# Optimization experiments

Measured on AMD Instinct MI355X. Metric: run time of the kernel, lower is better.

## Reference

```python
import jax, jax.numpy as jnp
import numpy as np

HIDDEN = 128

def setup_inputs() -> dict:
    key = jax.random.key(0)
    ks = jax.random.split(key, 7)
    B, T, I, O = 256, 512, 256, 1000
    s_ih = 1.0 / np.sqrt(HIDDEN)
    x = jax.random.normal(ks[0], (B, T, I), dtype=jnp.float32)
    W_ih = jax.random.uniform(ks[1], (HIDDEN, I), minval=-s_ih, maxval=s_ih, dtype=jnp.float32)
    W_hh = jax.random.uniform(ks[2], (HIDDEN, HIDDEN), minval=-s_ih, maxval=s_ih, dtype=jnp.float32)
    b_ih = jax.random.uniform(ks[3], (HIDDEN,), minval=-s_ih, maxval=s_ih, dtype=jnp.float32)
    b_hh = jax.random.uniform(ks[4], (HIDDEN,), minval=-s_ih, maxval=s_ih, dtype=jnp.float32)
    s_fc = 1.0 / np.sqrt(HIDDEN)
    W_fc = jax.random.uniform(ks[5], (O, HIDDEN), minval=-s_fc, maxval=s_fc, dtype=jnp.float32)
    b_fc = jax.random.uniform(ks[6], (O,), minval=-s_fc, maxval=s_fc, dtype=jnp.float32)
    return {"x": x, "W_ih": W_ih, "W_hh": W_hh, "b_ih": b_ih, "b_hh": b_hh, "W_fc": W_fc, "b_fc": b_fc}


def reference(x, W_ih, W_hh, b_ih, b_hh, W_fc, b_fc):
    B = x.shape[0]
    # Precompute input projection for all timesteps in one big GEMM: [B,T,H]
    xp = jnp.einsum('bti,hi->bth', x, W_ih) + b_ih + b_hh
    h0 = jnp.zeros((B, HIDDEN), dtype=x.dtype)

    def step(h, xp_t):
        h = jnp.tanh(xp_t + h @ W_hh.T)
        return h, None

    # scan over time axis; only the final hidden state feeds the fc head
    h_last, _ = jax.lax.scan(step, h0, jnp.swapaxes(xp, 0, 1))
    return h_last @ W_fc.T + b_fc
```

## Files before the change

kernel.cpp:

```cpp
#include <hip/hip_runtime.h>


#define HID    128
#define TSTEPS 512
#define BATCH  256
#define INDIM  256
#define ODIM   1000

typedef _Float16 f16x8 __attribute__((ext_vector_type(8)));
typedef __fp16   fp16x2 __attribute__((ext_vector_type(2)));
typedef float    f32x4 __attribute__((ext_vector_type(4)));

__device__ __forceinline__ unsigned pk16(float a, float b) {
    union { fp16x2 h; unsigned u; } t;
    t.h = __builtin_amdgcn_cvt_pkrtz(a, b);
    return t.u;
}
__device__ __forceinline__ float tanh_fast(float v) {
    float e = __expf(2.f * v);
    float r = __builtin_amdgcn_rcpf(e + 1.f);
    return __builtin_fmaf(-2.f, r, 1.f);
}

__global__ __launch_bounds__(256) void k_phase1(const float* __restrict__ x,
                                                const float* __restrict__ Wih,
                                                const float* __restrict__ bih,
                                                const float* __restrict__ bhh,
                                                float* __restrict__ xp) {
    __shared__ __align__(16) _Float16 xs[2][4096];
    __shared__ __align__(16) _Float16 wsm[2][4096];

    const int tid  = threadIdx.x;
    const int wave = tid >> 6, lane = tid & 63;
    const int quad = lane >> 4, l16 = lane & 15;
    const int wm = wave >> 1, wn = wave & 1;
    const int m0 = blockIdx.x * 128;

    int srow[4], scol[4], sdst[4];
#pragma unroll
    for (int q = 0; q < 4; q++) {
        int li = q * 256 + tid;
        srow[q] = li >> 3;
        scol[q] = li & 7;
        sdst[q] = srow[q] * 32 + ((((scol[q] >> 1) ^ srow[q]) & 3) << 3) + ((scol[q] & 1) << 2);
    }

    float bias_v[4];
#pragma unroll
    for (int nt = 0; nt < 4; nt++) {
        int j = wn * 64 + nt * 16 + l16;
        bias_v[nt] = bih[j] + bhh[j];
    }

    float4 rx[4], rw[4];
#define LOAD_STAGE(KC)                                                              \
    {                                                                               \
        _Pragma("unroll") for (int q = 0; q < 4; q++) {                             \
            rx[q] = *(const float4*)(x + (size_t)(m0 + srow[q]) * INDIM + (KC) * 32 + scol[q] * 4); \
            rw[q] = *(const float4*)(Wih + (size_t)srow[q] * INDIM + (KC) * 32 + scol[q] * 4);      \
        }                                                                           \
    }
#define WRITE_STAGE(BUF)                                                            \
    {                                                                               \
        _Pragma("unroll") for (int q = 0; q < 4; q++) {                             \
            uint2 px, pw;                                                           \
            px.x = pk16(rx[q].x, rx[q].y); px.y = pk16(rx[q].z, rx[q].w);           \
            pw.x = pk16(rw[q].x, rw[q].y); pw.y = pk16(rw[q].z, rw[q].w);           \
            *(uint2*)&xs[BUF][sdst[q]]  = px;                                       \
            *(uint2*)&wsm[BUF][sdst[q]] = pw;                                       \
        }                                                                           \
    }

    f32x4 acc[4][4];
#pragma unroll
    for (int mt = 0; mt < 4; mt++)
#pragma unroll
        for (int nt = 0; nt < 4; nt++) {
            acc[mt][nt].x = 0.f; acc[mt][nt].y = 0.f;
            acc[mt][nt].z = 0.f; acc[mt][nt].w = 0.f;
        }

    LOAD_STAGE(0);
    WRITE_STAGE(0);
    __syncthreads();

    for (int kc = 0; kc < 8; kc++) {
        const int b = kc & 1;
        if (kc < 7) LOAD_STAGE(kc + 1);

        f16x8 a[4], bw[4];
#pragma unroll
        for (int mt = 0; mt < 4; mt++) {
            int row = wm * 64 + mt * 16 + l16;
            a[mt] = *(const f16x8*)&xs[b][row * 32 + (((quad ^ row) & 3) << 3)];
        }
#pragma unroll
        for (int nt = 0; nt < 4; nt++) {
            int row = wn * 64 + nt * 16 + l16;
            bw[nt] = *(const f16x8*)&wsm[b][row * 32 + (((quad ^ row) & 3) << 3)];
        }
#pragma unroll
        for (int mt = 0; mt < 4; mt++)
#pragma unroll
            for (int nt = 0; nt < 4; nt++)
                acc[mt][nt] = __builtin_amdgcn_mfma_f32_16x16x32_f16(a[mt], bw[nt], acc[mt][nt], 0, 0, 0);

        if (kc < 7) WRITE_STAGE(b ^ 1);
        __syncthreads();
    }

#pragma unroll
    for (int mt = 0; mt < 4; mt++)
#pragma unroll
        for (int nt = 0; nt < 4; nt++)
#pragma unroll
            for (int reg = 0; reg < 4; reg++) {
                int row = m0 + wm * 64 + mt * 16 + quad * 4 + reg;
                xp[(size_t)row * HID + wn * 64 + nt * 16 + l16] = acc[mt][nt][reg] + bias_v[nt];
            }
#undef LOAD_STAGE
#undef WRITE_STAGE
}

#define RNN_STEP4(TV, XQI, XQC, PB) {                                             \
    _Pragma("unroll") for (int reg = 0; reg < 4; reg++) {                         \
        float hv = tanh_fast(C[reg]);                                             \
        int m = quad * 4 + reg;                                                   \
        hp[PB][m * 128 + ((((jbase >> 3) ^ m) & 15) << 3) + (jbase & 7)] =        \
            (_Float16)hv;                                                         \
    }                                                                             \
    if ((TV) + 4 < TSTEPS) {                                                      \
        _Pragma("unroll") for (int reg = 0; reg < 4; reg++)                       \
            XQI[reg] = xpb[ib[reg] + ((TV) + 4) * HID];                           \
    }                                                                             \
    asm volatile("s_waitcnt lgkmcnt(0)\n\ts_barrier" ::: "memory");               \
    f16x8 A[4];                                                                   \
    _Pragma("unroll") for (int kc = 0; kc < 4; kc++)                              \
        A[kc] = *(const f16x8*)&hp[PB][l16 * 128 + ((((kc * 4 + quad) ^ l16) & 15) << 3)]; \
    f32x4 ch, cl;                                                                 \
    ch.x = XQC[0]; ch.y = XQC[1]; ch.z = XQC[2]; ch.w = XQC[3];                   \
    cl.x = 0.f; cl.y = 0.f; cl.z = 0.f; cl.w = 0.f;                               \
    ch = __builtin_amdgcn_mfma_f32_16x16x32_f16(A[0], Bf[0], ch, 0, 0, 0);        \
    cl = __builtin_amdgcn_mfma_f32_16x16x32_f16(A[2], Bf[2], cl, 0, 0, 0);        \
    ch = __builtin_amdgcn_mfma_f32_16x16x32_f16(A[1], Bf[1], ch, 0, 0, 0);        \
    cl = __builtin_amdgcn_mfma_f32_16x16x32_f16(A[3], Bf[3], cl, 0, 0, 0);        \
    C = ch + cl;                                                                  \
}

__global__ __launch_bounds__(512) void k_rnn4(const float* __restrict__ Whh,
                                              float* __restrict__ ws) {
    __shared__ __align__(16) _Float16 hp[2][16 * 128];
    const int tid  = threadIdx.x;
    const int wave = tid >> 6, lane = tid & 63;
    const int quad = lane >> 4, l16 = lane & 15;
    const int r0    = blockIdx.x * 16;
    const int jbase = wave * 16 + l16;

    f16x8 Bf[4];
#pragma unroll
    for (int kc = 0; kc < 4; kc++) {
        const float* p = Whh + (size_t)jbase * HID + kc * 32 + quad * 8;
        float4 e0 = *(const float4*)p, e1 = *(const float4*)(p + 4);
        union { unsigned u[4]; f16x8 v; } t;
        t.u[0] = pk16(e0.x, e0.y); t.u[1] = pk16(e0.z, e0.w);
        t.u[2] = pk16(e1.x, e1.y); t.u[3] = pk16(e1.z, e1.w);
        Bf[kc] = t.v;
    }

    const float* xpb = ws;
    int ib[4];
#pragma unroll
    for (int reg = 0; reg < 4; reg++)
        ib[reg] = (r0 + quad * 4 + reg) * (TSTEPS * HID) + jbase;

    f32x4 C;
    float xq0[4], xq1[4], xq2[4], xq3[4];
    C.x = xpb[ib[0]]; C.y = xpb[ib[1]]; C.z = xpb[ib[2]]; C.w = xpb[ib[3]];
#pragma unroll
    for (int reg = 0; reg < 4; reg++) {
        xq1[reg] = xpb[ib[reg] + 1 * HID];
        xq2[reg] = xpb[ib[reg] + 2 * HID];
        xq3[reg] = xpb[ib[reg] + 3 * HID];
    }

    for (int t = 0; t < 508; t += 4) {
        RNN_STEP4(t,     xq0, xq1, 0);
        RNN_STEP4(t + 1, xq1, xq2, 1);
        RNN_STEP4(t + 2, xq2, xq3, 0);
        RNN_STEP4(t + 3, xq3, xq0, 1);
    }
    RNN_STEP4(508, xq0, xq1, 0);
    RNN_STEP4(509, xq1, xq2, 1);
    RNN_STEP4(510, xq2, xq3, 0);

#pragma unroll
    for (int reg = 0; reg < 4; reg++)
        ws[ib[reg]] = tanh_fast(C[reg]);
}

__global__ __launch_bounds__(256) void k_fc(const float* __restrict__ ws,
                                            const float* __restrict__ Wfc,
                                            const float* __restrict__ bfc,
                                            float* __restrict__ out) {
    __shared__ float hb[HID];
    const int b   = blockIdx.x;
    const int tid = threadIdx.x;
    if (tid < HID) hb[tid] = ws[(size_t)b * (TSTEPS * HID) + tid];
    __syncthreads();

    for (int o = tid; o < ODIM; o += 256) {
        const float* wr = Wfc + (size_t)o * HID;
        float acc = 0.f;
#pragma unroll
        for (int q = 0; q < 32; q++) {
            float4 wv = *(const float4*)(wr + q * 4);
            float4 hv = *(const float4*)&hb[q * 4];
            acc += wv.x * hv.x + wv.y * hv.y + wv.z * hv.z + wv.w * hv.w;
        }
        out[(size_t)b * ODIM + o] = acc + bfc[o];
    }
}

extern "C" void kernel_launch(void* const* d_in, const int* in_sizes, int n_in,
                              void* d_out, int out_size, void* d_ws, size_t ws_size,
                              hipStream_t stream) {
    const float* x   = (const float*)d_in[0];
    const float* Wih = (const float*)d_in[1];
    const float* Whh = (const float*)d_in[2];
    const float* bih = (const float*)d_in[3];
    const float* bhh = (const float*)d_in[4];
    const float* Wfc = (const float*)d_in[5];
    const float* bfc = (const float*)d_in[6];
    float* out = (float*)d_out;
    float* ws  = (float*)d_ws;

    k_phase1<<<dim3(1024), dim3(256), 0, stream>>>(x, Wih, bih, bhh, ws);
    k_rnn4  <<<dim3(16),   dim3(512), 0, stream>>>(Whh, ws);
    k_fc    <<<dim3(BATCH), dim3(256), 0, stream>>>(ws, Wfc, bfc, out);
}
```

Before: 392.6 us.

## Swap MFMA operand order to get row-contiguous accumulators and vectorized IO

Swaps the A/B operands of the MFMA in both the input-projection GEMM and the recurrent step, so each lane's accumulator holds 4 consecutive hidden columns of one batch row. Phase-1 can then store xp with 16-byte vector stores and load the bias as vectors. In the recurrence, the per-step xp prefetch becomes one float4 load instead of 4 strided scalar loads, and the h writeback to LDS becomes one packed 8-byte store instead of 4 scalar half stores. Precomputed LDS addresses drop per-step index arithmetic. The recurrence stays latency-bound by barriers and MFMA chains, so the gain depends on how much the scalar loads and stores sat on the critical path.

```diff
diff --git a/kernel.cpp b/kernel.cpp
--- a/kernel.cpp
+++ b/kernel.cpp
@@ -45,11 +45,11 @@
         sdst[q] = srow[q] * 32 + ((((scol[q] >> 1) ^ srow[q]) & 3) << 3) + ((scol[q] & 1) << 2);
     }
 
-    float bias_v[4];
+    f32x4 bias_v[4];
 #pragma unroll
     for (int nt = 0; nt < 4; nt++) {
-        int j = wn * 64 + nt * 16 + l16;
-        bias_v[nt] = bih[j] + bhh[j];
+        int j0 = wn * 64 + nt * 16 + quad * 4;
+        bias_v[nt] = *(const f32x4*)(bih + j0) + *(const f32x4*)(bhh + j0);
     }
 
     float4 rx[4], rw[4];
@@ -103,47 +103,43 @@
         for (int mt = 0; mt < 4; mt++)
 #pragma unroll
             for (int nt = 0; nt < 4; nt++)
-                acc[mt][nt] = __builtin_amdgcn_mfma_f32_16x16x32_f16(a[mt], bw[nt], acc[mt][nt], 0, 0, 0);
+                acc[mt][nt] = __builtin_amdgcn_mfma_f32_16x16x32_f16(bw[nt], a[mt], acc[mt][nt], 0, 0, 0);
 
         if (kc < 7) WRITE_STAGE(b ^ 1);
         __syncthreads();
     }
 
 #pragma unroll
-    for (int mt = 0; mt < 4; mt++)
-#pragma unroll
-        for (int nt = 0; nt < 4; nt++)
-#pragma unroll
-            for (int reg = 0; reg < 4; reg++) {
-                int row = m0 + wm * 64 + mt * 16 + quad * 4 + reg;
-                xp[(size_t)row * HID + wn * 64 + nt * 16 + l16] = acc[mt][nt][reg] + bias_v[nt];
-            }
+    for (int mt = 0; mt < 4; mt++) {
+        int row = m0 + wm * 64 + mt * 16 + l16;
+#pragma unroll
+        for (int nt = 0; nt < 4; nt++) {
+            int col = wn * 64 + nt * 16 + quad * 4;
+            *(f32x4*)&xp[(size_t)row * HID + col] = acc[mt][nt] + bias_v[nt];
+        }
+    }
 #undef LOAD_STAGE
 #undef WRITE_STAGE
 }
 
 #define RNN_STEP4(TV, XQI, XQC, PB) {                                             \
-    _Pragma("unroll") for (int reg = 0; reg < 4; reg++) {                         \
-        float hv = tanh_fast(C[reg]);                                             \
-        int m = quad * 4 + reg;                                                   \
-        hp[PB][m * 128 + ((((jbase >> 3) ^ m) & 15) << 3) + (jbase & 7)] =        \
-            (_Float16)hv;                                                         \
-    }                                                                             \
-    if ((TV) + 4 < TSTEPS) {                                                      \
-        _Pragma("unroll") for (int reg = 0; reg < 4; reg++)                       \
-            XQI[reg] = xpb[ib[reg] + ((TV) + 4) * HID];                           \
-    }                                                                             \
+    uint2 pw;                                                                     \
+    pw.x = pk16(tanh_fast(C.x), tanh_fast(C.y));                                  \
+    pw.y = pk16(tanh_fast(C.z), tanh_fast(C.w));                                  \
+    *(uint2*)&hp[PB][waddr] = pw;                                                 \
+    if ((TV) + 4 < TSTEPS)                                                        \
+        XQI = *(const f32x4*)(xpb + ((TV) + 4) * HID);                            \
     asm volatile("s_waitcnt lgkmcnt(0)\n\ts_barrier" ::: "memory");               \
-    f16x8 A[4];                                                                   \
-    _Pragma("unroll") for (int kc = 0; kc < 4; kc++)                              \
-        A[kc] = *(const f16x8*)&hp[PB][l16 * 128 + ((((kc * 4 + quad) ^ l16) & 15) << 3)]; \
-    f32x4 ch, cl;                                                                 \
-    ch.x = XQC[0]; ch.y = XQC[1]; ch.z = XQC[2]; ch.w = XQC[3];                   \
+    f16x8 H0 = *(const f16x8*)&hp[PB][raddr0];                                    \
+    f16x8 H1 = *(const f16x8*)&hp[PB][raddr1];                                    \
+    f16x8 H2 = *(const f16x8*)&hp[PB][raddr2];                                    \
+    f16x8 H3 = *(const f16x8*)&hp[PB][raddr3];                                    \
+    f32x4 ch = XQC, cl;                                                           \
     cl.x = 0.f; cl.y = 0.f; cl.z = 0.f; cl.w = 0.f;                               \
-    ch = __builtin_amdgcn_mfma_f32_16x16x32_f16(A[0], Bf[0], ch, 0, 0, 0);        \
-    cl = __builtin_amdgcn_mfma_f32_16x16x32_f16(A[2], Bf[2], cl, 0, 0, 0);        \
-    ch = __builtin_amdgcn_mfma_f32_16x16x32_f16(A[1], Bf[1], ch, 0, 0, 0);        \
-    cl = __builtin_amdgcn_mfma_f32_16x16x32_f16(A[3], Bf[3], cl, 0, 0, 0);        \
+    ch = __builtin_amdgcn_mfma_f32_16x16x32_f16(Wf[0], H0, ch, 0, 0, 0);          \
+    cl = __builtin_amdgcn_mfma_f32_16x16x32_f16(Wf[2], H2, cl, 0, 0, 0);          \
+    ch = __builtin_amdgcn_mfma_f32_16x16x32_f16(Wf[1], H1, ch, 0, 0, 0);          \
+    cl = __builtin_amdgcn_mfma_f32_16x16x32_f16(Wf[3], H3, cl, 0, 0, 0);          \
     C = ch + cl;                                                                  \
 }
 
@@ -153,35 +149,32 @@
     const int tid  = threadIdx.x;
     const int wave = tid >> 6, lane = tid & 63;
     const int quad = lane >> 4, l16 = lane & 15;
-    const int r0    = blockIdx.x * 16;
-    const int jbase = wave * 16 + l16;
-
-    f16x8 Bf[4];
+    const int r0   = blockIdx.x * 16;
+
+    f16x8 Wf[4];
 #pragma unroll
     for (int kc = 0; kc < 4; kc++) {
-        const float* p = Whh + (size_t)jbase * HID + kc * 32 + quad * 8;
+        const float* p = Whh + (size_t)(16 * wave + l16) * HID + kc * 32 + quad * 8;
         float4 e0 = *(const float4*)p, e1 = *(const float4*)(p + 4);
         union { unsigned u[4]; f16x8 v; } t;
         t.u[0] = pk16(e0.x, e0.y); t.u[1] = pk16(e0.z, e0.w);
         t.u[2] = pk16(e1.x, e1.y); t.u[3] = pk16(e1.z, e1.w);
-        Bf[kc] = t.v;
-    }
-
-    const float* xpb = ws;
-    int ib[4];
-#pragma unroll
-    for (int reg = 0; reg < 4; reg++)
-        ib[reg] = (r0 + quad * 4 + reg) * (TSTEPS * HID) + jbase;
-
-    f32x4 C;
-    float xq0[4], xq1[4], xq2[4], xq3[4];
-    C.x = xpb[ib[0]]; C.y = xpb[ib[1]]; C.z = xpb[ib[2]]; C.w = xpb[ib[3]];
-#pragma unroll
-    for (int reg = 0; reg < 4; reg++) {
-        xq1[reg] = xpb[ib[reg] + 1 * HID];
-        xq2[reg] = xpb[ib[reg] + 2 * HID];
-        xq3[reg] = xpb[ib[reg] + 3 * HID];
-    }
+        Wf[kc] = t.v;
+    }
+
+    const int raddr0 = l16 * 128 + ((((0 * 4 + quad) ^ l16) & 15) << 3);
+    const int raddr1 = l16 * 128 + ((((1 * 4 + quad) ^ l16) & 15) << 3);
+    const int raddr2 = l16 * 128 + ((((2 * 4 + quad) ^ l16) & 15) << 3);
+    const int raddr3 = l16 * 128 + ((((3 * 4 + quad) ^ l16) & 15) << 3);
+    const int waddr  = l16 * 128 + ((((2 * wave + (quad >> 1)) ^ l16) & 15) << 3) + ((quad & 1) << 2);
+
+    const float* xpb = ws + (size_t)(r0 + l16) * (TSTEPS * HID) + 16 * wave + 4 * quad;
+
+    f32x4 C, xq0, xq1, xq2, xq3;
+    C   = *(const f32x4*)(xpb);
+    xq1 = *(const f32x4*)(xpb + 1 * HID);
+    xq2 = *(const f32x4*)(xpb + 2 * HID);
+    xq3 = *(const f32x4*)(xpb + 3 * HID);
 
     for (int t = 0; t < 508; t += 4) {
         RNN_STEP4(t,     xq0, xq1, 0);
@@ -193,10 +186,12 @@
     RNN_STEP4(509, xq1, xq2, 1);
     RNN_STEP4(510, xq2, xq3, 0);
 
-#pragma unroll
-    for (int reg = 0; reg < 4; reg++)
-        ws[ib[reg]] = tanh_fast(C[reg]);
-}
+    f32x4 o;
+    o.x = tanh_fast(C.x); o.y = tanh_fast(C.y);
+    o.z = tanh_fast(C.z); o.w = tanh_fast(C.w);
+    *(f32x4*)(ws + (size_t)(r0 + l16) * (TSTEPS * HID) + 16 * wave + 4 * quad) = o;
+}
+#undef RNN_STEP4
 
 __global__ __launch_bounds__(256) void k_fc(const float* __restrict__ ws,
                                             const float* __restrict__ Wfc,
```

After: 375.4 us. -4.4%, faster.
